# Kernel optimization log

Measured on AMD Instinct MI355X. Metric: run time of the kernel, lower is better.

The kernel has to match this reference:

```python
import jax, jax.numpy as jnp
import numpy as np

# hyperparameters (see init_kwargs)
DP, DS, DO, D, K, C = 256, 256, 64, 320, 10, 10
SI, NS = 100, 22
ALIGN = 0.05
COEF = 0.3989422917366028  # 1/sqrt(2*pi)
B, SEQ, T_STEPS = 32, 512, 200


def _linear_params(key, fan_in, fan_out):
    # torch nn.Linear default init: U(-1/sqrt(fan_in), 1/sqrt(fan_in))
    s = 1.0 / np.sqrt(fan_in)
    kw, kb = jax.random.split(key)
    w = jax.random.uniform(kw, (fan_in, fan_out), minval=-s, maxval=s, dtype=jnp.float32)
    b = jax.random.uniform(kb, (fan_out,), minval=-s, maxval=s, dtype=jnp.float32)
    return w, b


def setup_inputs() -> dict:
    key = jax.random.key(0)
    ks = jax.random.split(key, 8)
    sentence = jax.random.randint(ks[0], (B, SEQ), 0, SI)
    speaker_id = jax.random.randint(ks[1], (B,), 0, NS)
    Lut_P = jax.random.normal(ks[2], (SI, DP), dtype=jnp.float32)
    Lut_S = jax.random.normal(ks[3], (NS, DS), dtype=jnp.float32)
    Na_w, Na_b = _linear_params(ks[4], D * K, 3 * C)
    Nu_w, Nu_b = _linear_params(ks[5], D * K, D)
    No_w, No_b = _linear_params(ks[6], D * K, DO)
    kf = jax.random.split(ks[7], 2)
    Fu_w, Fu_b = _linear_params(kf[0], DS, DP)
    Fo_w, Fo_b = _linear_params(kf[1], DS, D * K)
    return dict(sentence=sentence, speaker_id=speaker_id, Lut_P=Lut_P, Lut_S=Lut_S,
                Na_w=Na_w, Na_b=Na_b, Nu_w=Nu_w, Nu_b=Nu_b, No_w=No_w, No_b=No_b,
                Fu_w=Fu_w, Fu_b=Fu_b, Fo_w=Fo_w, Fo_b=Fo_b, T=T_STEPS)


def reference(sentence, speaker_id, Lut_P, Lut_S, Na_w, Na_b, Nu_w, Nu_b,
              No_w, No_b, Fu_w, Fu_b, Fo_w, Fo_b, T):
    batch, seq_len = sentence.shape
    # Encoder: embedding lookups
    lut_p = Lut_P[sentence]          # (B, S, dp)
    ident = Lut_S[speaker_id]        # (B, ds)

    # ident-dependent terms are loop-invariant; hoist out of the scan
    idt = jnp.tanh(ident @ Fu_w + Fu_b)   # (B, dp)
    fo = ident @ Fo_w + Fo_b              # (B, d*k)

    # initialize(): buffer seeded with speaker embedding in first dp rows
    S0 = jnp.zeros((batch, D, K), dtype=lut_p.dtype)
    S0 = S0.at[:, :DP, :].set(ident[:, :, None])
    mu0 = jnp.zeros((batch, C), dtype=lut_p.dtype)
    o0 = jnp.zeros((batch, DO), dtype=lut_p.dtype)

    J = jnp.arange(1, seq_len + 1, dtype=lut_p.dtype)  # (S,)

    def step(carry, _):
        S_tm1, mu_tm1, o_tm1 = carry
        # --- GMM attention ---
        out = (S_tm1.reshape(batch, D * K) @ Na_w + Na_b).reshape(batch, 3, C)
        k_t, b_t, y_t = out[:, 0], out[:, 1], out[:, 2]
        mu_t = mu_tm1 + ALIGN * jnp.exp(k_t)            # (B, c)
        sig_t = jnp.exp(b_t)                            # (B, c)
        g_t = jax.nn.softmax(y_t, axis=1)               # (B, c)
        # phi: (B, c, S)
        phi = g_t[:, :, None] * jnp.exp(-0.5 * sig_t[:, :, None] * (mu_t[:, :, None] - J) ** 2)
        alpha = COEF * phi.sum(axis=1)                  # (B, S)
        c_t = jnp.einsum('bs,bsd->bd', alpha, lut_p)    # (B, dp)
        # --- Decoder buffer update ---
        C_t = jnp.concatenate([c_t + idt, o_tm1 / 30.0], axis=1)        # (B, d)
        Sp = jnp.concatenate([C_t[:, :, None], S_tm1[:, :, :-1]], axis=2)  # (B, d, k)
        u = Sp.reshape(batch, D * K) @ Nu_w + Nu_b                      # (B, d)
        S_t = jnp.concatenate([u[:, :, None], S_tm1[:, :, :-1]], axis=2)
        o_t = (S_t.reshape(batch, D * K) + fo) @ No_w + No_b            # (B, do)
        return (S_t, mu_t, o_t), o_t

    (_, _, _), outs = jax.lax.scan(step, (S0, mu0, o0), None, length=T)
    return outs  # (T, B, do)
```

## Files before the change

### kernel.cpp

```cpp
#include <hip/hip_runtime.h>

#define DP   256
#define DD   320
#define KK   10
#define CC   10
#define DOUT 64
#define SEQn 512
#define BB   32
#define SI   100
#define NSL  32
#define NGR  8
#define BPG  4
#define NTH  640
#define DPS  10
#define RPS  100

#define PSA   448
#define UF_O  0
#define ZA_O  40
#define ZO_O  168
#define HALF_A (NGR*NSL*PSA)
#define PSB   320

typedef float f4 __attribute__((ext_vector_type(4)));

__device__ __forceinline__ void llc_ld(f4* dst, const float* p) {
    f4 r;
    asm volatile("global_load_dwordx4 %0, %1, off sc0 sc1" : "=&v"(r) : "v"(p));
    asm volatile("s_waitcnt vmcnt(0)" ::: "memory");
    __builtin_amdgcn_sched_barrier(0);
    *dst = r;
}
__device__ __forceinline__ void llc_st(float* p, f4 v) {
    asm volatile("global_store_dwordx4 %0, %1, off sc0 sc1" :: "v"(p), "v"(v) : "memory");
}

__global__ void prep_kernel(int* ctr) {
    if (threadIdx.x < 256) ctr[threadIdx.x] = 0;
}

__device__ __forceinline__ void gbar(int* c, int target) {
    asm volatile("s_waitcnt vmcnt(0)" ::: "memory");
    __syncthreads();
    if (threadIdx.x == 0) {
        __hip_atomic_fetch_add(c, 1, __ATOMIC_RELEASE, __HIP_MEMORY_SCOPE_AGENT);
        while (__hip_atomic_load(c, __ATOMIC_RELAXED, __HIP_MEMORY_SCOPE_AGENT) < target)
            __builtin_amdgcn_s_sleep(2);
    }
    __syncthreads();
}

__global__ __launch_bounds__(NTH) void recur_kernel(
    const int* __restrict__ sentence, const int* __restrict__ speaker,
    const float* __restrict__ LutP, const float* __restrict__ LutS,
    const float* __restrict__ NaW,  const float* __restrict__ NaB,
    const float* __restrict__ NuW,  const float* __restrict__ NuB,
    const float* __restrict__ NoW,  const float* __restrict__ NoB,
    const float* __restrict__ FuW,  const float* __restrict__ FuB,
    const float* __restrict__ FoW,  const float* __restrict__ FoB,
    float* __restrict__ ws, const int* __restrict__ Tptr,
    float* __restrict__ out)
{
    const int tid  = threadIdx.x;
    const int s    = blockIdx.x & (NSL - 1);
    const int g    = blockIdx.x >> 5;
    const bool owner = (s < BPG);
    const int dbase = s * DPS;
    const int rbase = s * RPS;
    int*  ctr  = (int*)ws + g * 32;
    float* pubA = ws + 256;
    float* pubB = ws + 256 + 2 * HALF_A;

    const int c_   = tid >> 6;
    const int lane = tid & 63;

    __shared__ float xsE[BPG][3328];
    __shared__ float wNa[RPS][32];
    __shared__ float wNo[RPS][65];
    __shared__ float naT0[DPS][32];
    __shared__ float noT0[DPS][65];
    __shared__ float identsh[BPG][DP];
    __shared__ float ufull[BPG][DD];
    __shared__ float colL[BPG][DD];
    __shared__ float ucol[BPG*DPS];
    __shared__ float zr[BPG*32];
    __shared__ float zor[BPG*DOUT];
    __shared__ float zastage[NSL][32];
    __shared__ float zostage[NSL][DOUT];
    __shared__ float fos[BPG][RPS];
    __shared__ float nubO[DPS];
    __shared__ float nabL[32];
    __shared__ float aoutL[32];
    __shared__ float muL[CC], sgL[CC], ggL[CC];
    __shared__ float alphaL[SEQn];
    __shared__ float histL[SI];
    __shared__ float idtF[DP];
    __shared__ float colF[DD];
    __shared__ float o_own[DOUT];
    __shared__ float foNoL[DOUT];
    __shared__ int   sentL[SEQn];
    __shared__ int   posidx[SEQn];
    __shared__ int   vstart[SI + 1];
    __shared__ int   vcnt[SI];

    for (int i = tid; i < RPS * 30; i += NTH) {
        int r = i / 30, c = i % 30;
        wNa[r][c] = NaW[(rbase + r) * 30 + c];
    }
    for (int i = tid; i < RPS * 64; i += NTH) {
        int r = i / 64, o = i % 64;
        wNo[r][o] = NoW[(rbase + r) * 64 + o];
    }
    if (tid < DPS * 30) { int dl = tid / 30, c = tid % 30; naT0[dl][c] = NaW[((dbase + dl) * KK) * 30 + c]; }
    if (tid < DPS * 64) { int dl = tid >> 6, o = tid & 63; noT0[dl][o] = NoW[((dbase + dl) * KK) * 64 + o]; }
    if (tid < DPS) nubO[tid] = NuB[dbase + tid];
    if (tid >= 16 && tid < 48) { int c = tid - 16; nabL[c] = (c < 30) ? NaB[c] : 0.f; }
    for (int i = tid; i < BPG * DP; i += NTH) {
        int j = i / DP, v = i % DP;
        identsh[j][v] = LutS[speaker[g * BPG + j] * DP + v];
    }
    __syncthreads();

    float w[50];
    #pragma unroll
    for (int q = 0; q < 50; ++q)
        w[q] = NuW[(size_t)(lane * 50 + q) * DD + dbase + c_];

    for (int i = tid; i < BPG * RPS; i += NTH) {
        int j = i / RPS, r = i % RPS;
        float acc = FoB[rbase + r];
        for (int v = 0; v < DP; v += 8) {
            float wv[8];
            #pragma unroll
            for (int e = 0; e < 8; ++e) wv[e] = FoW[(v + e) * 3200 + rbase + r];
            #pragma unroll
            for (int e = 0; e < 8; ++e) acc += identsh[j][v + e] * wv[e];
        }
        fos[j][r] = acc;
    }
    if (owner) {
        if (tid < DP) {
            float acc = FuB[tid];
            for (int v = 0; v < DP; v += 8) {
                float wv[8];
                #pragma unroll
                for (int e = 0; e < 8; ++e) wv[e] = FuW[(v + e) * DP + tid];
                #pragma unroll
                for (int e = 0; e < 8; ++e) acc += identsh[s][v + e] * wv[e];
            }
            idtF[tid] = tanhf(acc);
        }
        if (tid >= 512 && tid < 512 + CC) muL[tid - 512] = 0.f;
        if (tid < SEQn) sentL[tid] = sentence[(g * BPG + s) * SEQn + tid];
        __syncthreads();
        if (tid < SI) { int cnt = 0; for (int q = 0; q < SEQn; ++q) if (sentL[q] == tid) ++cnt; vcnt[tid] = cnt; }
        __syncthreads();
        if (tid == 0) { int run = 0; for (int v = 0; v < SI; ++v) { vstart[v] = run; run += vcnt[v]; } vstart[SI] = run; }
        __syncthreads();
        if (tid < SI) { int k = vstart[tid]; for (int q = 0; q < SEQn; ++q) if (sentL[q] == tid) posidx[k++] = q; }
    }
    for (int i = tid; i < BPG * 3200; i += NTH) {
        int j = i / 3200, row = i % 3200;
        int d = row / KK;
        xsE[j][(row / 50) * 52 + (row % 50)] = (d < DP) ? identsh[j][d] : 0.f;
    }
    __syncthreads();
    if (tid < 128) {
        int j = tid >> 5, c = tid & 31;
        float acc = 0.f;
        if (c < 30)
            for (int rr = 0; rr < RPS; ++rr) {
                int row = rbase + rr;
                acc += xsE[j][(row / 50) * 52 + (row % 50)] * wNa[rr][c];
            }
        zr[j * 32 + c] = acc;
    }
    if (tid >= 128 && tid < 384) {
        int t = tid - 128, j = t >> 6, o = t & 63;
        float acc = 0.f;
        for (int rr = 0; rr < RPS; ++rr) acc += fos[j][rr] * wNo[rr][o];
        zor[j * 64 + o] = acc;
    }
    __syncthreads();
    {
        float* pa0 = pubA + (g * NSL + s) * PSA;
        if (tid < 32) llc_st(pa0 + ZA_O + tid * 4, *(f4*)&zr[tid * 4]);
        if (tid >= 32 && tid < 96) { int q = tid - 32; llc_st(pa0 + ZO_O + q * 4, *(f4*)&zor[q * 4]); }
    }
    gbar(ctr, 32 * 1);

    const int T = Tptr[0];

    for (int i = 0; i < T; ++i) {
        const int rh = i & 1, wh = rh ^ 1;
        float* pa_r = pubA + rh * HALF_A + g * NSL * PSA;
        float* pa_w = pubA + wh * HALF_A + (g * NSL + s) * PSA;

        if (i > 0 && tid < 320) {
            int p = tid / 10, q = tid % 10;
            f4 v; llc_ld(&v, pa_r + p * PSA + UF_O + q * 4);
            #pragma unroll
            for (int e = 0; e < 4; ++e) {
                int f = q * 4 + e;
                ufull[f / 10][p * 10 + (f % 10)] = v[e];
            }
        }
        __syncthreads();

        if (owner) {
            if (tid < 256) {
                int p = tid >> 3, q = tid & 7;
                f4 v; llc_ld(&v, pa_r + p * PSA + ZA_O + s * 32 + q * 4);
                #pragma unroll
                for (int e = 0; e < 4; ++e) zastage[p][q * 4 + e] = v[e];
            }
            if (tid < 512) {
                int p = tid >> 4, q = tid & 15;
                f4 v; llc_ld(&v, pa_r + p * PSA + ZO_O + s * 64 + q * 4);
                #pragma unroll
                for (int e = 0; e < 4; ++e) zostage[p][q * 4 + e] = v[e];
            }
            __syncthreads();
            if (tid < 30) {
                float a = nabL[tid];
                for (int p = 0; p < NSL; ++p) a += zastage[p][tid];
                aoutL[tid] = a;
            }
            if (tid >= 64 && tid < 128) {
                int o = tid - 64;
                float v = 0.f;
                for (int p = 0; p < NSL; ++p) v += zostage[p][o];
                if (i == 0) { foNoL[o] = NoB[o] + v; o_own[o] = 0.f; }
                else        o_own[o] = foNoL[o] + v;
            }
            __syncthreads();
            if (tid < CC) {
                muL[tid] += 0.05f * expf(aoutL[tid]);
                sgL[tid] = expf(aoutL[10 + tid]);
                float m = -1e30f;
                for (int q = 0; q < CC; ++q) m = fmaxf(m, aoutL[20 + q]);
                float ssum = 0.f;
                for (int q = 0; q < CC; ++q) ssum += expf(aoutL[20 + q] - m);
                ggL[tid] = expf(aoutL[20 + tid] - m) / ssum;
            }
            __syncthreads();
            if (tid < SEQn) {
                float J = (float)(tid + 1);
                float a = 0.f;
                #pragma unroll
                for (int c = 0; c < CC; ++c) { float dm = muL[c] - J; a += ggL[c] * __expf(-0.5f * sgL[c] * dm * dm); }
                alphaL[tid] = a * 0.3989422917366028f;
            }
            __syncthreads();
            if (tid < SI) {
                float h = 0.f;
                for (int k = vstart[tid]; k < vstart[tid + 1]; ++k) h += alphaL[posidx[k]];
                histL[tid] = h;
            }
            __syncthreads();
            if (tid < DP) {
                float acc = idtF[tid];
                for (int v = 0; v < SI; v += 10) {
                    float wv[10];
                    #pragma unroll
                    for (int e = 0; e < 10; ++e) wv[e] = LutP[(v + e) * DP + tid];
                    #pragma unroll
                    for (int e = 0; e < 10; ++e) acc += histL[v + e] * wv[e];
                }
                colF[tid] = acc;
            } else if (tid < DD) {
                colF[tid] = o_own[tid - DP] * (1.0f / 30.0f);
            }
            __syncthreads();
            if (i > 0 && tid < DOUT)
                out[((size_t)(i - 1) * BB + (g * BPG + s)) * DOUT + tid] = o_own[tid];
            if (tid < 80) llc_st(pubB + (g * BPG + s) * PSB + tid * 4, *(f4*)&colF[tid * 4]);
        }

        for (int it = tid; it < BPG * DD; it += NTH) {
            int j = it / DD, d = it % DD;
            float* p = &xsE[j][(d / 5) * 52 + (d % 5) * 10];
            float t0 = p[0];
            float v1 = p[1], v2 = p[2], v3 = p[3], v4 = p[4], v5 = p[5], v6 = p[6], v7 = p[7], v8 = p[8];
            p[1] = (i == 0) ? t0 : ufull[j][d];
            p[2] = v1; p[3] = v2; p[4] = v3; p[5] = v4; p[6] = v5; p[7] = v6; p[8] = v7; p[9] = v8;
        }
        gbar(ctr, 32 * (2 * i + 2));

        if (tid < 320) {
            int j = tid / 80, q = tid % 80;
            f4 v; llc_ld(&v, pubB + (g * BPG + j) * PSB + q * 4);
            #pragma unroll
            for (int e = 0; e < 4; ++e) colL[j][q * 4 + e] = v[e];
        }
        __syncthreads();
        for (int it = tid; it < BPG * DD; it += NTH) {
            int j = it / DD, d = it % DD;
            xsE[j][(d / 5) * 52 + (d % 5) * 10] = colL[j][d];
        }
        __syncthreads();

        {
            float accE[BPG];
            #pragma unroll
            for (int j = 0; j < BPG; ++j) {
                const float* xb = &xsE[j][lane * 52];
                float a = 0.f;
                #pragma unroll
                for (int qq = 0; qq < 12; ++qq) {
                    f4 x = *(const f4*)(xb + qq * 4);
                    a += x.x * w[qq * 4] + x.y * w[qq * 4 + 1] + x.z * w[qq * 4 + 2] + x.w * w[qq * 4 + 3];
                }
                a += xb[48] * w[48] + xb[49] * w[49];
                accE[j] = a;
            }
            #pragma unroll
            for (int j = 0; j < BPG; ++j)
                for (int off = 32; off; off >>= 1) accE[j] += __shfl_xor(accE[j], off, 64);
            if (lane == 0) {
                #pragma unroll
                for (int j = 0; j < BPG; ++j) ucol[j * DPS + c_] = accE[j] + nubO[c_];
            }
        }
        __syncthreads();

        if (tid < 128) {
            int j = tid >> 5, c = tid & 31;
            float acc = 0.f;
            if (c < 30) {
                for (int dd = 0; dd < DPS; ++dd) {
                    int rg = 2 * s + (dd >= 5);
                    int of = dd * 10 - (dd >= 5 ? 50 : 0);
                    const float* xb = &xsE[j][rg * 52 + of];
                    #pragma unroll
                    for (int k = 1; k < KK; ++k) acc += xb[k] * wNa[dd * 10 + k][c];
                }
                #pragma unroll
                for (int dl = 0; dl < DPS; ++dl) acc += ucol[j * DPS + dl] * naT0[dl][c];
            }
            zr[j * 32 + c] = acc;
        }
        if (tid >= 128 && tid < 384) {
            int t = tid - 128, j = t >> 6, o = t & 63;
            float acc = 0.f;
            for (int dd = 0; dd < DPS; ++dd) {
                int rg = 2 * s + (dd >= 5);
                int of = dd * 10 - (dd >= 5 ? 50 : 0);
                const float* xb = &xsE[j][rg * 52 + of];
                #pragma unroll
                for (int k = 1; k < KK; ++k) acc += xb[k] * wNo[dd * 10 + k][o];
            }
            #pragma unroll
            for (int dl = 0; dl < DPS; ++dl) acc += ucol[j * DPS + dl] * noT0[dl][o];
            zor[j * 64 + o] = acc;
        }
        __syncthreads();

        if (tid < 10)                llc_st(pa_w + UF_O + tid * 4,        *(f4*)&ucol[tid * 4]);
        if (tid >= 10 && tid < 42)  { int q = tid - 10; llc_st(pa_w + ZA_O + q * 4, *(f4*)&zr[q * 4]); }
        if (tid >= 42 && tid < 106) { int q = tid - 42; llc_st(pa_w + ZO_O + q * 4, *(f4*)&zor[q * 4]); }
        gbar(ctr, 32 * (2 * i + 3));
    }

    if (owner) {
        float* pa_r = pubA + (T & 1) * HALF_A + g * NSL * PSA;
        if (tid < 512) {
            int p = tid >> 4, q = tid & 15;
            f4 v; llc_ld(&v, pa_r + p * PSA + ZO_O + s * 64 + q * 4);
            #pragma unroll
            for (int e = 0; e < 4; ++e) zostage[p][q * 4 + e] = v[e];
        }
        __syncthreads();
        if (tid < DOUT) {
            float v = foNoL[tid];
            for (int p = 0; p < NSL; ++p) v += zostage[p][tid];
            out[((size_t)(T - 1) * BB + (g * BPG + s)) * DOUT + tid] = v;
        }
    }
}

extern "C" void kernel_launch(void* const* d_in, const int* in_sizes, int n_in,
                              void* d_out, int out_size, void* d_ws, size_t ws_size,
                              hipStream_t stream) {
    const int*   sentence = (const int*)d_in[0];
    const int*   speaker  = (const int*)d_in[1];
    const float* LutP = (const float*)d_in[2];
    const float* LutS = (const float*)d_in[3];
    const float* NaW  = (const float*)d_in[4];
    const float* NaB  = (const float*)d_in[5];
    const float* NuW  = (const float*)d_in[6];
    const float* NuB  = (const float*)d_in[7];
    const float* NoW  = (const float*)d_in[8];
    const float* NoB  = (const float*)d_in[9];
    const float* FuW  = (const float*)d_in[10];
    const float* FuB  = (const float*)d_in[11];
    const float* FoW  = (const float*)d_in[12];
    const float* FoB  = (const float*)d_in[13];
    const int*   Tptr = (const int*)d_in[14];
    float* ws   = (float*)d_ws;
    float* outp = (float*)d_out;

    hipLaunchKernelGGL(prep_kernel, dim3(1), dim3(256), 0, stream, (int*)d_ws);
    hipLaunchKernelGGL(recur_kernel, dim3(NSL * NGR), dim3(NTH), 0, stream,
                       sentence, speaker, LutP, LutS, NaW, NaB,
                       NuW, NuB, NoW, NoB, FuW, FuB, FoW, FoB,
                       ws, Tptr, outp);
}
```

Before: 5.343 ms.

## Replace mid-step grid barrier with per-owner flags and overlap Nu dot product

Drops one of the two per-step group barriers. Each owner block now publishes its context column and sets a per-owner flag, and consumers spin on those four flags instead. While waiting, every block computes the part of the Nu matmul that covers the shifted buffer history, then adds only the new column's contribution once it arrives. It also batches the pubA loads into one wait, switches to an unpadded xsE layout, and uses an epoch-flag barrier so waiters poll a flag rather than the counter. The risks are subtle memory-ordering bugs in the flag handoff and higher register use from the 50-entry shifted weight array.

```diff
diff --git a/kernel.cpp b/kernel.cpp
--- a/kernel.cpp
+++ b/kernel.cpp
@@ -21,6 +21,8 @@
 #define ZO_O  168
 #define HALF_A (NGR*NSL*PSA)
 #define PSB   320
+#define PUBA_OFF 1024
+#define PUBB_OFF (PUBA_OFF + 2*HALF_A)
 
 typedef float f4 __attribute__((ext_vector_type(4)));
 
@@ -36,16 +38,18 @@
 }
 
 __global__ void prep_kernel(int* ctr) {
-    if (threadIdx.x < 256) ctr[threadIdx.x] = 0;
-}
-
-__device__ __forceinline__ void gbar(int* c, int target) {
+    if (threadIdx.x < 1024) ctr[threadIdx.x] = 0;
+}
+
+__device__ __forceinline__ void barrier_ep(int* C, int* F, int epoch) {
     asm volatile("s_waitcnt vmcnt(0)" ::: "memory");
     __syncthreads();
     if (threadIdx.x == 0) {
-        __hip_atomic_fetch_add(c, 1, __ATOMIC_RELEASE, __HIP_MEMORY_SCOPE_AGENT);
-        while (__hip_atomic_load(c, __ATOMIC_RELAXED, __HIP_MEMORY_SCOPE_AGENT) < target)
-            __builtin_amdgcn_s_sleep(2);
+        int pos = __hip_atomic_fetch_add(C, 1, __ATOMIC_RELEASE, __HIP_MEMORY_SCOPE_AGENT);
+        if (pos == 32 * epoch - 1)
+            __hip_atomic_store(F, epoch, __ATOMIC_RELEASE, __HIP_MEMORY_SCOPE_AGENT);
+        while (__hip_atomic_load(F, __ATOMIC_RELAXED, __HIP_MEMORY_SCOPE_AGENT) < epoch)
+            __builtin_amdgcn_s_sleep(4);
     }
     __syncthreads();
 }
@@ -67,67 +71,63 @@
     const bool owner = (s < BPG);
     const int dbase = s * DPS;
     const int rbase = s * RPS;
-    int*  ctr  = (int*)ws + g * 32;
-    float* pubA = ws + 256;
-    float* pubB = ws + 256 + 2 * HALF_A;
+    int* ip = (int*)ws;
+    int* Cc = ip + g * 32;
+    int* Ff = ip + 256 + g * 32;
+    int* CF = ip + 512 + g * 32;
+    float* pubA = ws + PUBA_OFF;
+    float* pubB = ws + PUBB_OFF;
 
     const int c_   = tid >> 6;
     const int lane = tid & 63;
 
-    __shared__ float xsE[BPG][3328];
+    __shared__ float xsE[BPG][3200];
     __shared__ float wNa[RPS][32];
-    __shared__ float wNo[RPS][65];
-    __shared__ float naT0[DPS][32];
-    __shared__ float noT0[DPS][65];
-    __shared__ float identsh[BPG][DP];
+    __shared__ float wNo[RPS][64];
+    __shared__ float nuT0[DPS][DD];
+    __shared__ float zastage[NSL][32];
+    __shared__ float zostage[NSL][64];
     __shared__ float ufull[BPG][DD];
     __shared__ float colL[BPG][DD];
-    __shared__ float ucol[BPG*DPS];
+    __shared__ float colF[DD];
+    __shared__ float ucolL[BPG*DPS];
     __shared__ float zr[BPG*32];
     __shared__ float zor[BPG*DOUT];
-    __shared__ float zastage[NSL][32];
-    __shared__ float zostage[NSL][DOUT];
+    __shared__ float alphaL[SEQn];
+    __shared__ float histL[SI];
+    __shared__ float identsh[BPG][DP];
     __shared__ float fos[BPG][RPS];
-    __shared__ float nubO[DPS];
-    __shared__ float nabL[32];
+    __shared__ float idtF[DP];
+    __shared__ float o_ownL[DOUT];
+    __shared__ float foNoL[DOUT];
     __shared__ float aoutL[32];
     __shared__ float muL[CC], sgL[CC], ggL[CC];
-    __shared__ float alphaL[SEQn];
-    __shared__ float histL[SI];
-    __shared__ float idtF[DP];
-    __shared__ float colF[DD];
-    __shared__ float o_own[DOUT];
-    __shared__ float foNoL[DOUT];
+    __shared__ float nubO[DPS];
     __shared__ int   sentL[SEQn];
     __shared__ int   posidx[SEQn];
     __shared__ int   vstart[SI + 1];
     __shared__ int   vcnt[SI];
 
-    for (int i = tid; i < RPS * 30; i += NTH) {
-        int r = i / 30, c = i % 30;
-        wNa[r][c] = NaW[(rbase + r) * 30 + c];
-    }
-    for (int i = tid; i < RPS * 64; i += NTH) {
-        int r = i / 64, o = i % 64;
+    for (int idx = tid; idx < RPS * 32; idx += NTH) {
+        int r = idx >> 5, c = idx & 31;
+        wNa[r][c] = (c < 30) ? NaW[(rbase + r) * 30 + c] : 0.f;
+    }
+    for (int idx = tid; idx < RPS * 64; idx += NTH) {
+        int r = idx >> 6, o = idx & 63;
         wNo[r][o] = NoW[(rbase + r) * 64 + o];
     }
-    if (tid < DPS * 30) { int dl = tid / 30, c = tid % 30; naT0[dl][c] = NaW[((dbase + dl) * KK) * 30 + c]; }
-    if (tid < DPS * 64) { int dl = tid >> 6, o = tid & 63; noT0[dl][o] = NoW[((dbase + dl) * KK) * 64 + o]; }
+    for (int idx = tid; idx < DPS * DD; idx += NTH) {
+        int cl = idx / DD, d = idx % DD;
+        nuT0[cl][d] = NuW[(size_t)(d * 10) * DD + dbase + cl];
+    }
     if (tid < DPS) nubO[tid] = NuB[dbase + tid];
-    if (tid >= 16 && tid < 48) { int c = tid - 16; nabL[c] = (c < 30) ? NaB[c] : 0.f; }
-    for (int i = tid; i < BPG * DP; i += NTH) {
-        int j = i / DP, v = i % DP;
+    for (int idx = tid; idx < BPG * DP; idx += NTH) {
+        int j = idx / DP, v = idx % DP;
         identsh[j][v] = LutS[speaker[g * BPG + j] * DP + v];
     }
     __syncthreads();
-
-    float w[50];
-    #pragma unroll
-    for (int q = 0; q < 50; ++q)
-        w[q] = NuW[(size_t)(lane * 50 + q) * DD + dbase + c_];
-
-    for (int i = tid; i < BPG * RPS; i += NTH) {
-        int j = i / RPS, r = i % RPS;
+    for (int idx = tid; idx < BPG * RPS; idx += NTH) {
+        int j = idx / RPS, r = idx % RPS;
         float acc = FoB[rbase + r];
         for (int v = 0; v < DP; v += 8) {
             float wv[8];
@@ -152,86 +152,114 @@
         }
         if (tid >= 512 && tid < 512 + CC) muL[tid - 512] = 0.f;
         if (tid < SEQn) sentL[tid] = sentence[(g * BPG + s) * SEQn + tid];
-        __syncthreads();
+    }
+    for (int idx = tid; idx < BPG * 3200; idx += NTH) {
+        int j = idx / 3200, r = idx % 3200;
+        int d = r / KK;
+        xsE[j][r] = (d < DP) ? identsh[j][d] : 0.f;
+    }
+    __syncthreads();
+    if (owner) {
         if (tid < SI) { int cnt = 0; for (int q = 0; q < SEQn; ++q) if (sentL[q] == tid) ++cnt; vcnt[tid] = cnt; }
         __syncthreads();
         if (tid == 0) { int run = 0; for (int v = 0; v < SI; ++v) { vstart[v] = run; run += vcnt[v]; } vstart[SI] = run; }
         __syncthreads();
         if (tid < SI) { int k = vstart[tid]; for (int q = 0; q < SEQn; ++q) if (sentL[q] == tid) posidx[k++] = q; }
     }
-    for (int i = tid; i < BPG * 3200; i += NTH) {
-        int j = i / 3200, row = i % 3200;
-        int d = row / KK;
-        xsE[j][(row / 50) * 52 + (row % 50)] = (d < DP) ? identsh[j][d] : 0.f;
-    }
-    __syncthreads();
+    float wE[50];
+    #pragma unroll
+    for (int m = 0; m < 12; ++m) {
+        #pragma unroll
+        for (int e = 0; e < 4; ++e) {
+            int r = 256 * m + lane * 4 + e;
+            wE[m * 4 + e] = (r % 10 == 9) ? 0.f : NuW[(size_t)(r + 1) * DD + dbase + c_];
+        }
+    }
+    #pragma unroll
+    for (int e = 0; e < 2; ++e) {
+        int r = 3072 + lane * 2 + e;
+        wE[48 + e] = (r % 10 == 9) ? 0.f : NuW[(size_t)(r + 1) * DD + dbase + c_];
+    }
     if (tid < 128) {
         int j = tid >> 5, c = tid & 31;
-        float acc = 0.f;
-        if (c < 30)
-            for (int rr = 0; rr < RPS; ++rr) {
-                int row = rbase + rr;
-                acc += xsE[j][(row / 50) * 52 + (row % 50)] * wNa[rr][c];
-            }
-        zr[j * 32 + c] = acc;
+        float a = 0.f;
+        if (c < 30) for (int rr = 0; rr < RPS; ++rr) a += xsE[j][rbase + rr] * wNa[rr][c];
+        zr[j * 32 + c] = a;
     }
     if (tid >= 128 && tid < 384) {
         int t = tid - 128, j = t >> 6, o = t & 63;
-        float acc = 0.f;
-        for (int rr = 0; rr < RPS; ++rr) acc += fos[j][rr] * wNo[rr][o];
-        zor[j * 64 + o] = acc;
+        float a = 0.f;
+        for (int rr = 0; rr < RPS; ++rr) a += fos[j][rr] * wNo[rr][o];
+        zor[j * 64 + o] = a;
     }
     __syncthreads();
     {
-        float* pa0 = pubA + (g * NSL + s) * PSA;
-        if (tid < 32) llc_st(pa0 + ZA_O + tid * 4, *(f4*)&zr[tid * 4]);
-        if (tid >= 32 && tid < 96) { int q = tid - 32; llc_st(pa0 + ZO_O + q * 4, *(f4*)&zor[q * 4]); }
-    }
-    gbar(ctr, 32 * 1);
+        float* pa0 = pubA + (size_t)(g * NSL + s) * PSA;
+        if (tid >= 16 && tid < 48)  { int q = tid - 16; llc_st(pa0 + ZA_O + q * 4, *(f4*)&zr[q * 4]); }
+        if (tid >= 48 && tid < 112) { int q = tid - 48; llc_st(pa0 + ZO_O + q * 4, *(f4*)&zor[q * 4]); }
+    }
+    barrier_ep(Cc, Ff, 1);
 
     const int T = Tptr[0];
 
     for (int i = 0; i < T; ++i) {
-        const int rh = i & 1, wh = rh ^ 1;
-        float* pa_r = pubA + rh * HALF_A + g * NSL * PSA;
-        float* pa_w = pubA + wh * HALF_A + (g * NSL + s) * PSA;
-
-        if (i > 0 && tid < 320) {
-            int p = tid / 10, q = tid % 10;
-            f4 v; llc_ld(&v, pa_r + p * PSA + UF_O + q * 4);
-            #pragma unroll
-            for (int e = 0; e < 4; ++e) {
-                int f = q * 4 + e;
-                ufull[f / 10][p * 10 + (f % 10)] = v[e];
+        {
+            const float* pa_r = pubA + (size_t)(i & 1) * HALF_A + (size_t)g * NSL * PSA;
+            f4 v_uf = {0,0,0,0}, v_za = {0,0,0,0}, v_zo = {0,0,0,0};
+            bool h_uf = false, h_za = false, h_zo = false;
+            if (i > 0 && tid < 320) {
+                const float* p = pa_r + (tid / 10) * PSA + UF_O + (tid % 10) * 4;
+                asm volatile("global_load_dwordx4 %0, %1, off sc0 sc1" : "=&v"(v_uf) : "v"(p));
+                h_uf = true;
+            }
+            if (owner) {
+                if (tid >= 320 && tid < 576) {
+                    int t = tid - 320;
+                    const float* p = pa_r + (t >> 3) * PSA + ZA_O + s * 32 + (t & 7) * 4;
+                    asm volatile("global_load_dwordx4 %0, %1, off sc0 sc1" : "=&v"(v_za) : "v"(p));
+                    h_za = true;
+                }
+                if (tid < 512) {
+                    const float* p = pa_r + (tid >> 4) * PSA + ZO_O + s * 64 + (tid & 15) * 4;
+                    asm volatile("global_load_dwordx4 %0, %1, off sc0 sc1" : "=&v"(v_zo) : "v"(p));
+                    h_zo = true;
+                }
+            }
+            asm volatile("s_waitcnt vmcnt(0)" ::: "memory");
+            __builtin_amdgcn_sched_barrier(0);
+            if (h_uf) {
+                int p = tid / 10, q = tid % 10;
+                #pragma unroll
+                for (int e = 0; e < 4; ++e) { int f = q * 4 + e; ufull[f / 10][p * 10 + f % 10] = v_uf[e]; }
+            }
+            if (h_za) { int t = tid - 320; *(f4*)&zastage[t >> 3][(t & 7) * 4] = v_za; }
+            if (h_zo) { *(f4*)&zostage[tid >> 4][(tid & 15) * 4] = v_zo; }
+        }
+        __syncthreads();
+        if (i > 0) {
+            for (int it = tid; it < BPG * DD; it += NTH) {
+                int j = it / DD, d = it % DD;
+                float* p = &xsE[j][d * 10];
+                float t0 = p[0], t1 = p[1], t2 = p[2], t3 = p[3], t4 = p[4],
+                      t5 = p[5], t6 = p[6], t7 = p[7], t8 = p[8];
+                p[0] = ufull[j][d];
+                p[1] = t0; p[2] = t1; p[3] = t2; p[4] = t3; p[5] = t4;
+                p[6] = t5; p[7] = t6; p[8] = t7; p[9] = t8;
             }
         }
         __syncthreads();
 
         if (owner) {
-            if (tid < 256) {
-                int p = tid >> 3, q = tid & 7;
-                f4 v; llc_ld(&v, pa_r + p * PSA + ZA_O + s * 32 + q * 4);
-                #pragma unroll
-                for (int e = 0; e < 4; ++e) zastage[p][q * 4 + e] = v[e];
-            }
-            if (tid < 512) {
-                int p = tid >> 4, q = tid & 15;
-                f4 v; llc_ld(&v, pa_r + p * PSA + ZO_O + s * 64 + q * 4);
-                #pragma unroll
-                for (int e = 0; e < 4; ++e) zostage[p][q * 4 + e] = v[e];
-            }
-            __syncthreads();
             if (tid < 30) {
-                float a = nabL[tid];
+                float a = NaB[tid];
                 for (int p = 0; p < NSL; ++p) a += zastage[p][tid];
                 aoutL[tid] = a;
-            }
-            if (tid >= 64 && tid < 128) {
+            } else if (tid >= 64 && tid < 128) {
                 int o = tid - 64;
                 float v = 0.f;
                 for (int p = 0; p < NSL; ++p) v += zostage[p][o];
-                if (i == 0) { foNoL[o] = NoB[o] + v; o_own[o] = 0.f; }
-                else        o_own[o] = foNoL[o] + v;
+                if (i == 0) { foNoL[o] = NoB[o] + v; o_ownL[o] = 0.f; }
+                else        o_ownL[o] = foNoL[o] + v;
             }
             __syncthreads();
             if (tid < CC) {
@@ -269,106 +297,99 @@
                 }
                 colF[tid] = acc;
             } else if (tid < DD) {
-                colF[tid] = o_own[tid - DP] * (1.0f / 30.0f);
+                colF[tid] = o_ownL[tid - DP] * (1.0f / 30.0f);
             }
             __syncthreads();
             if (i > 0 && tid < DOUT)
-                out[((size_t)(i - 1) * BB + (g * BPG + s)) * DOUT + tid] = o_own[tid];
-            if (tid < 80) llc_st(pubB + (g * BPG + s) * PSB + tid * 4, *(f4*)&colF[tid * 4]);
-        }
-
-        for (int it = tid; it < BPG * DD; it += NTH) {
-            int j = it / DD, d = it % DD;
-            float* p = &xsE[j][(d / 5) * 52 + (d % 5) * 10];
-            float t0 = p[0];
-            float v1 = p[1], v2 = p[2], v3 = p[3], v4 = p[4], v5 = p[5], v6 = p[6], v7 = p[7], v8 = p[8];
-            p[1] = (i == 0) ? t0 : ufull[j][d];
-            p[2] = v1; p[3] = v2; p[4] = v3; p[5] = v4; p[6] = v5; p[7] = v6; p[8] = v7; p[9] = v8;
-        }
-        gbar(ctr, 32 * (2 * i + 2));
-
+                out[((size_t)(i - 1) * BB + (g * BPG + s)) * DOUT + tid] = o_ownL[tid];
+            if (tid < 80) llc_st(pubB + (size_t)(g * BPG + s) * PSB + tid * 4, *(f4*)&colF[tid * 4]);
+            asm volatile("s_waitcnt vmcnt(0)" ::: "memory");
+            __syncthreads();
+            if (tid == 0)
+                __hip_atomic_store(&CF[s], i + 1, __ATOMIC_RELEASE, __HIP_MEMORY_SCOPE_AGENT);
+        }
+
+        float acc[BPG];
+        #pragma unroll
+        for (int j = 0; j < BPG; ++j) {
+            const float* xb = &xsE[j][0];
+            float a = 0.f;
+            #pragma unroll
+            for (int m = 0; m < 12; ++m) {
+                f4 x = *(const f4*)(xb + 256 * m + lane * 4);
+                a += x.x * wE[m * 4] + x.y * wE[m * 4 + 1] + x.z * wE[m * 4 + 2] + x.w * wE[m * 4 + 3];
+            }
+            {
+                float x0 = xb[3072 + lane * 2], x1 = xb[3072 + lane * 2 + 1];
+                a += x0 * wE[48] + x1 * wE[49];
+            }
+            acc[j] = a;
+        }
+
+        if (tid < BPG) {
+            while (__hip_atomic_load(&CF[tid], __ATOMIC_RELAXED, __HIP_MEMORY_SCOPE_AGENT) < i + 1)
+                __builtin_amdgcn_s_sleep(2);
+        }
+        __syncthreads();
         if (tid < 320) {
-            int j = tid / 80, q = tid % 80;
-            f4 v; llc_ld(&v, pubB + (g * BPG + j) * PSB + q * 4);
-            #pragma unroll
-            for (int e = 0; e < 4; ++e) colL[j][q * 4 + e] = v[e];
-        }
-        __syncthreads();
-        for (int it = tid; it < BPG * DD; it += NTH) {
-            int j = it / DD, d = it % DD;
-            xsE[j][(d / 5) * 52 + (d % 5) * 10] = colL[j][d];
-        }
-        __syncthreads();
-
-        {
-            float accE[BPG];
-            #pragma unroll
-            for (int j = 0; j < BPG; ++j) {
-                const float* xb = &xsE[j][lane * 52];
-                float a = 0.f;
-                #pragma unroll
-                for (int qq = 0; qq < 12; ++qq) {
-                    f4 x = *(const f4*)(xb + qq * 4);
-                    a += x.x * w[qq * 4] + x.y * w[qq * 4 + 1] + x.z * w[qq * 4 + 2] + x.w * w[qq * 4 + 3];
-                }
-                a += xb[48] * w[48] + xb[49] * w[49];
-                accE[j] = a;
-            }
-            #pragma unroll
-            for (int j = 0; j < BPG; ++j)
-                for (int off = 32; off; off >>= 1) accE[j] += __shfl_xor(accE[j], off, 64);
-            if (lane == 0) {
-                #pragma unroll
-                for (int j = 0; j < BPG; ++j) ucol[j * DPS + c_] = accE[j] + nubO[c_];
-            }
+            f4 v; llc_ld(&v, pubB + (size_t)(g * BPG + tid / 80) * PSB + (tid % 80) * 4);
+            *(f4*)&colL[tid / 80][(tid % 80) * 4] = v;
+        }
+        __syncthreads();
+
+        #pragma unroll
+        for (int j = 0; j < BPG; ++j) {
+            float a = acc[j];
+            #pragma unroll
+            for (int m = 0; m < 5; ++m) { int d = lane + 64 * m; a += colL[j][d] * nuT0[c_][d]; }
+            #pragma unroll
+            for (int off = 32; off; off >>= 1) a += __shfl_xor(a, off, 64);
+            if (lane == 0) ucolL[j * DPS + c_] = a + nubO[c_];
         }
         __syncthreads();
 
         if (tid < 128) {
             int j = tid >> 5, c = tid & 31;
-            float acc = 0.f;
+            float a = 0.f;
             if (c < 30) {
                 for (int dd = 0; dd < DPS; ++dd) {
-                    int rg = 2 * s + (dd >= 5);
-                    int of = dd * 10 - (dd >= 5 ? 50 : 0);
-                    const float* xb = &xsE[j][rg * 52 + of];
+                    const float* xb = &xsE[j][(dbase + dd) * 10];
                     #pragma unroll
-                    for (int k = 1; k < KK; ++k) acc += xb[k] * wNa[dd * 10 + k][c];
+                    for (int k = 0; k < 9; ++k) a += xb[k] * wNa[dd * 10 + k + 1][c];
                 }
                 #pragma unroll
-                for (int dl = 0; dl < DPS; ++dl) acc += ucol[j * DPS + dl] * naT0[dl][c];
-            }
-            zr[j * 32 + c] = acc;
+                for (int dl = 0; dl < DPS; ++dl) a += ucolL[j * DPS + dl] * wNa[dl * 10][c];
+            }
+            zr[j * 32 + c] = a;
         }
         if (tid >= 128 && tid < 384) {
             int t = tid - 128, j = t >> 6, o = t & 63;
-            float acc = 0.f;
+            float a = 0.f;
             for (int dd = 0; dd < DPS; ++dd) {
-                int rg = 2 * s + (dd >= 5);
-                int of = dd * 10 - (dd >= 5 ? 50 : 0);
-                const float* xb = &xsE[j][rg * 52 + of];
-                #pragma unroll
-                for (int k = 1; k < KK; ++k) acc += xb[k] * wNo[dd * 10 + k][o];
-            }
-            #pragma unroll
-            for (int dl = 0; dl < DPS; ++dl) acc += ucol[j * DPS + dl] * noT0[dl][o];
-            zor[j * 64 + o] = acc;
-        }
-        __syncthreads();
-
-        if (tid < 10)                llc_st(pa_w + UF_O + tid * 4,        *(f4*)&ucol[tid * 4]);
-        if (tid >= 10 && tid < 42)  { int q = tid - 10; llc_st(pa_w + ZA_O + q * 4, *(f4*)&zr[q * 4]); }
-        if (tid >= 42 && tid < 106) { int q = tid - 42; llc_st(pa_w + ZO_O + q * 4, *(f4*)&zor[q * 4]); }
-        gbar(ctr, 32 * (2 * i + 3));
+                const float* xb = &xsE[j][(dbase + dd) * 10];
+                #pragma unroll
+                for (int k = 0; k < 9; ++k) a += xb[k] * wNo[dd * 10 + k + 1][o];
+            }
+            #pragma unroll
+            for (int dl = 0; dl < DPS; ++dl) a += ucolL[j * DPS + dl] * wNo[dl * 10][o];
+            zor[j * 64 + o] = a;
+        }
+        __syncthreads();
+
+        {
+            float* pa_w = pubA + (size_t)((i + 1) & 1) * HALF_A + (size_t)(g * NSL + s) * PSA;
+            if (tid < 10)                     llc_st(pa_w + UF_O + tid * 4, *(f4*)&ucolL[tid * 4]);
+            else if (tid >= 16 && tid < 48)  { int q = tid - 16; llc_st(pa_w + ZA_O + q * 4, *(f4*)&zr[q * 4]); }
+            else if (tid >= 48 && tid < 112) { int q = tid - 48; llc_st(pa_w + ZO_O + q * 4, *(f4*)&zor[q * 4]); }
+        }
+        barrier_ep(Cc, Ff, i + 2);
     }
 
     if (owner) {
-        float* pa_r = pubA + (T & 1) * HALF_A + g * NSL * PSA;
+        const float* pa_r = pubA + (size_t)(T & 1) * HALF_A + (size_t)g * NSL * PSA;
         if (tid < 512) {
-            int p = tid >> 4, q = tid & 15;
-            f4 v; llc_ld(&v, pa_r + p * PSA + ZO_O + s * 64 + q * 4);
-            #pragma unroll
-            for (int e = 0; e < 4; ++e) zostage[p][q * 4 + e] = v[e];
+            f4 v; llc_ld(&v, pa_r + (tid >> 4) * PSA + ZO_O + s * 64 + (tid & 15) * 4);
+            *(f4*)&zostage[tid >> 4][(tid & 15) * 4] = v;
         }
         __syncthreads();
         if (tid < DOUT) {
@@ -400,7 +421,7 @@
     float* ws   = (float*)d_ws;
     float* outp = (float*)d_out;
 
-    hipLaunchKernelGGL(prep_kernel, dim3(1), dim3(256), 0, stream, (int*)d_ws);
+    hipLaunchKernelGGL(prep_kernel, dim3(1), dim3(1024), 0, stream, (int*)d_ws);
     hipLaunchKernelGGL(recur_kernel, dim3(NSL * NGR), dim3(NTH), 0, stream,
                        sentence, speaker, LutP, LutS, NaW, NaB,
                        NuW, NuB, NoW, NoB, FuW, FuB, FoW, FoB,
```

Measured after the change: 14.14 ms. 2.65x slower.

## Replace mid-step group barrier with per-owner ready flags and batch owner loads

Applied to the files above, without the earlier changes.

The full 32-block group barrier after the owner phase is replaced with per-owner release flags. Each non-owner block waits only on the four owner blocks whose column data it needs. The owner's two staged global loads are now issued together under a single waitcnt instead of serialising. The group barrier counter is adjusted to one increment per step, and workspace offsets are widened to size_t. This cuts one global barrier per recurrence step, at the cost of extra flag memory and relying on correct release/acquire ordering on the flags.

```diff
diff --git a/kernel.cpp b/kernel.cpp
--- a/kernel.cpp
+++ b/kernel.cpp
@@ -21,6 +21,7 @@
 #define ZO_O  168
 #define HALF_A (NGR*NSL*PSA)
 #define PSB   320
+#define CF_OFF 240000
 
 typedef float f4 __attribute__((ext_vector_type(4)));
 
@@ -36,7 +37,10 @@
 }
 
 __global__ void prep_kernel(int* ctr) {
-    if (threadIdx.x < 256) ctr[threadIdx.x] = 0;
+    if (threadIdx.x < 256) {
+        ctr[threadIdx.x] = 0;
+        ctr[CF_OFF + threadIdx.x] = 0;
+    }
 }
 
 __device__ __forceinline__ void gbar(int* c, int target) {
@@ -68,6 +72,7 @@
     const int dbase = s * DPS;
     const int rbase = s * RPS;
     int*  ctr  = (int*)ws + g * 32;
+    int*  CFg  = (int*)ws + CF_OFF + g * 32;
     float* pubA = ws + 256;
     float* pubB = ws + 256 + 2 * HALF_A;
 
@@ -183,7 +188,7 @@
     }
     __syncthreads();
     {
-        float* pa0 = pubA + (g * NSL + s) * PSA;
+        float* pa0 = pubA + (size_t)(g * NSL + s) * PSA;
         if (tid < 32) llc_st(pa0 + ZA_O + tid * 4, *(f4*)&zr[tid * 4]);
         if (tid >= 32 && tid < 96) { int q = tid - 32; llc_st(pa0 + ZO_O + q * 4, *(f4*)&zor[q * 4]); }
     }
@@ -193,8 +198,8 @@
 
     for (int i = 0; i < T; ++i) {
         const int rh = i & 1, wh = rh ^ 1;
-        float* pa_r = pubA + rh * HALF_A + g * NSL * PSA;
-        float* pa_w = pubA + wh * HALF_A + (g * NSL + s) * PSA;
+        float* pa_r = pubA + (size_t)rh * HALF_A + (size_t)g * NSL * PSA;
+        float* pa_w = pubA + (size_t)wh * HALF_A + (size_t)(g * NSL + s) * PSA;
 
         if (i > 0 && tid < 320) {
             int p = tid / 10, q = tid % 10;
@@ -208,18 +213,19 @@
         __syncthreads();
 
         if (owner) {
+            f4 v_za = {0.f,0.f,0.f,0.f}, v_zo = {0.f,0.f,0.f,0.f};
             if (tid < 256) {
-                int p = tid >> 3, q = tid & 7;
-                f4 v; llc_ld(&v, pa_r + p * PSA + ZA_O + s * 32 + q * 4);
-                #pragma unroll
-                for (int e = 0; e < 4; ++e) zastage[p][q * 4 + e] = v[e];
+                const float* p = pa_r + (tid >> 3) * PSA + ZA_O + s * 32 + (tid & 7) * 4;
+                asm volatile("global_load_dwordx4 %0, %1, off sc0 sc1" : "=&v"(v_za) : "v"(p));
             }
             if (tid < 512) {
-                int p = tid >> 4, q = tid & 15;
-                f4 v; llc_ld(&v, pa_r + p * PSA + ZO_O + s * 64 + q * 4);
-                #pragma unroll
-                for (int e = 0; e < 4; ++e) zostage[p][q * 4 + e] = v[e];
-            }
+                const float* p = pa_r + (tid >> 4) * PSA + ZO_O + s * 64 + (tid & 15) * 4;
+                asm volatile("global_load_dwordx4 %0, %1, off sc0 sc1" : "=&v"(v_zo) : "v"(p));
+            }
+            asm volatile("s_waitcnt vmcnt(0)" ::: "memory");
+            __builtin_amdgcn_sched_barrier(0);
+            if (tid < 256) *(f4*)&zastage[tid >> 3][(tid & 7) * 4] = v_za;
+            if (tid < 512) *(f4*)&zostage[tid >> 4][(tid & 15) * 4] = v_zo;
             __syncthreads();
             if (tid < 30) {
                 float a = nabL[tid];
@@ -274,7 +280,11 @@
             __syncthreads();
             if (i > 0 && tid < DOUT)
                 out[((size_t)(i - 1) * BB + (g * BPG + s)) * DOUT + tid] = o_own[tid];
-            if (tid < 80) llc_st(pubB + (g * BPG + s) * PSB + tid * 4, *(f4*)&colF[tid * 4]);
+            if (tid < 80) llc_st(pubB + (size_t)(g * BPG + s) * PSB + tid * 4, *(f4*)&colF[tid * 4]);
+            asm volatile("s_waitcnt vmcnt(0)" ::: "memory");
+            __syncthreads();
+            if (tid == 0)
+                __hip_atomic_store(&CFg[s], i + 1, __ATOMIC_RELEASE, __HIP_MEMORY_SCOPE_AGENT);
         }
 
         for (int it = tid; it < BPG * DD; it += NTH) {
@@ -285,11 +295,15 @@
             p[1] = (i == 0) ? t0 : ufull[j][d];
             p[2] = v1; p[3] = v2; p[4] = v3; p[5] = v4; p[6] = v5; p[7] = v6; p[8] = v7; p[9] = v8;
         }
-        gbar(ctr, 32 * (2 * i + 2));
+        if (tid < BPG) {
+            while (__hip_atomic_load(&CFg[tid], __ATOMIC_RELAXED, __HIP_MEMORY_SCOPE_AGENT) < i + 1)
+                __builtin_amdgcn_s_sleep(2);
+        }
+        __syncthreads();
 
         if (tid < 320) {
             int j = tid / 80, q = tid % 80;
-            f4 v; llc_ld(&v, pubB + (g * BPG + j) * PSB + q * 4);
+            f4 v; llc_ld(&v, pubB + (size_t)(g * BPG + j) * PSB + q * 4);
             #pragma unroll
             for (int e = 0; e < 4; ++e) colL[j][q * 4 + e] = v[e];
         }
@@ -359,16 +373,14 @@
         if (tid < 10)                llc_st(pa_w + UF_O + tid * 4,        *(f4*)&ucol[tid * 4]);
         if (tid >= 10 && tid < 42)  { int q = tid - 10; llc_st(pa_w + ZA_O + q * 4, *(f4*)&zr[q * 4]); }
         if (tid >= 42 && tid < 106) { int q = tid - 42; llc_st(pa_w + ZO_O + q * 4, *(f4*)&zor[q * 4]); }
-        gbar(ctr, 32 * (2 * i + 3));
+        gbar(ctr, 32 * (i + 2));
     }
 
     if (owner) {
-        float* pa_r = pubA + (T & 1) * HALF_A + g * NSL * PSA;
+        const float* pa_r = pubA + (size_t)(T & 1) * HALF_A + (size_t)g * NSL * PSA;
         if (tid < 512) {
-            int p = tid >> 4, q = tid & 15;
-            f4 v; llc_ld(&v, pa_r + p * PSA + ZO_O + s * 64 + q * 4);
-            #pragma unroll
-            for (int e = 0; e < 4; ++e) zostage[p][q * 4 + e] = v[e];
+            f4 v; llc_ld(&v, pa_r + (tid >> 4) * PSA + ZO_O + s * 64 + (tid & 15) * 4);
+            *(f4*)&zostage[tid >> 4][(tid & 15) * 4] = v;
         }
         __syncthreads();
         if (tid < DOUT) {
```

New measurement: 4.940 ms. 7.5% less time.
